# Kernel optimization log

Hardware: AMD Instinct MI355X
Metric: run time of the kernel (lower is better)

The kernel has to match this reference:

```python
import jax, jax.numpy as jnp
import numpy as np

B, N, IN_F, OUT_F, H, NUM_EDGE_TYPES = 16, 512, 256, 256, 8, 50
HEAD_DIM = OUT_F // H
LN_EPS = 1e-5


def setup_inputs() -> dict:
    key = jax.random.key(0)
    ks = jax.random.split(key, 8)
    x = jax.random.normal(ks[0], (B, N, IN_F), dtype=jnp.float32)
    adj = jax.random.randint(ks[1], (B, N, N), 0, 2, dtype=jnp.int32)
    edge_types = jax.random.randint(ks[2], (B, N, N), 0, NUM_EDGE_TYPES, dtype=jnp.int32)
    # Parameters (torch Linear stores weight as [out, in]; we keep [in, out] for x @ W)
    W = jax.random.normal(ks[3], (IN_F, OUT_F), dtype=jnp.float32) / np.sqrt(IN_F)
    a1 = jax.random.normal(ks[4], (HEAD_DIM,), dtype=jnp.float32) / np.sqrt(HEAD_DIM)
    a2 = jax.random.normal(ks[5], (HEAD_DIM,), dtype=jnp.float32) / np.sqrt(HEAD_DIM)
    edge_emb = jax.random.normal(ks[6], (NUM_EDGE_TYPES, H), dtype=jnp.float32) * 0.02
    edge_emb = edge_emb.at[0].set(0.0)  # padding_idx=0
    ln_gamma = jnp.ones((OUT_F,), dtype=jnp.float32)
    ln_beta = jnp.zeros((OUT_F,), dtype=jnp.float32)
    return {"x": x, "adj": adj, "edge_types": edge_types, "W": W, "a1": a1,
            "a2": a2, "edge_emb": edge_emb, "ln_gamma": ln_gamma, "ln_beta": ln_beta}


def reference(x, adj, edge_types, W, a1, a2, edge_emb, ln_gamma, ln_beta):
    Bx, Nx, _ = x.shape
    # Wh: [B, N, H, D]
    Wh = (x @ W).reshape(Bx, Nx, H, HEAD_DIM)
    # per-node attention scalars: [B, N, H]
    s1 = jnp.einsum('bnhd,d->bnh', Wh, a1)
    s2 = jnp.einsum('bnhd,d->bnh', Wh, a2)
    # e: [B, N(i), N(j), H]
    e = s1[:, :, None, :] + s2[:, None, :, :] + edge_emb[edge_types]
    e = jnp.where(e > 0, e, 0.2 * e)  # leaky_relu(0.2)
    e = jnp.where((adj == 0)[..., None], jnp.float32(-1e9), e)
    alpha = jax.nn.softmax(e, axis=2)  # softmax over j
    # (dropout omitted: eval mode / deterministic reference)
    h = jnp.einsum('bijh,bjhd->bihd', alpha, Wh).reshape(Bx, Nx, OUT_F)
    # LayerNorm over last dim
    mu = jnp.mean(h, axis=-1, keepdims=True)
    var = jnp.mean(jnp.square(h - mu), axis=-1, keepdims=True)
    hn = (h - mu) * jax.lax.rsqrt(var + LN_EPS) * ln_gamma + ln_beta
    return jax.nn.elu(hn)
```

## Files before the change

kernel.cpp:

```cpp
#include <hip/hip_runtime.h>
#include <hip/hip_bf16.h>
#include <stdint.h>

namespace gat {
constexpr int NB   = 16;
constexpr int NN   = 512;
constexpr int FIN  = 256;
constexpr int FOUT = 256;
constexpr int H    = 8;
constexpr int NE   = 50;
constexpr float L2E  = 1.4426950408889634f;
constexpr float MASKB = -192.0f;
constexpr float RBIAS = 0.00281502f;
}
using namespace gat;

typedef __attribute__((ext_vector_type(8))) short short8;
typedef __attribute__((ext_vector_type(4))) float f32x4;

__device__ __forceinline__ unsigned pk_bf16(unsigned ulo, unsigned uhi) {
  return __builtin_amdgcn_perm(uhi, ulo, 0x07060302u);
}
__device__ __forceinline__ unsigned pk2f(float a, float b) {
  return pk_bf16(__float_as_uint(a) + 0x8000u, __float_as_uint(b) + 0x8000u);
}
__device__ __forceinline__ unsigned short bf1(float a) {
  return (unsigned short)((__float_as_uint(a) + 0x8000u) >> 16);
}

__global__ __launch_bounds__(256) void k_prew(const float* __restrict__ Wm,
                                              const float* __restrict__ a1,
                                              const float* __restrict__ a2,
                                              unsigned short* __restrict__ WbTa) {
  const int blk = blockIdx.x;
  if (blk < 256) {
    const int k = blk;
    const int f = threadIdx.x;
    WbTa[f * FIN + k] = bf1(Wm[k * FOUT + f]);
  } else {
    const int k = threadIdx.x;
    const float* wr = Wm + (size_t)k * FOUT;
    #pragma unroll
    for (int h = 0; h < H; ++h) {
      float v1 = 0.f, v2 = 0.f;
      #pragma unroll
      for (int d = 0; d < 32; ++d) {
        const float wv = wr[h * 32 + d];
        v1 += wv * a1[d];
        v2 += wv * a2[d];
      }
      WbTa[(256 + h) * FIN + k] = bf1(v1);
      WbTa[(264 + h) * FIN + k] = bf1(v2);
    }
  }
}

__global__ __launch_bounds__(256, 4) void k_gp(
    const float* __restrict__ x, const unsigned short* __restrict__ WbTa,
    const int* __restrict__ adj, const int* __restrict__ ety,
    unsigned short* __restrict__ WhT, float* __restrict__ s1T, float* __restrict__ s2T,
    unsigned* __restrict__ codes)
{
  const int t = threadIdx.x;
  if (blockIdx.x >= 512) {
    const size_t base = ((size_t)(blockIdx.x - 512) * 256 + t) * 16;
    const int4* ap = (const int4*)(adj + base);
    const int4* ep = (const int4*)(ety + base);
    unsigned o[4];
    #pragma unroll
    for (int g = 0; g < 4; ++g) {
      const int4 a = ap[g];
      const int4 e = ep[g];
      o[g] = (unsigned)(e.x | (a.x << 6))
           | ((unsigned)(e.y | (a.y << 6)) << 8)
           | ((unsigned)(e.z | (a.z << 6)) << 16)
           | ((unsigned)(e.w | (a.w << 6)) << 24);
    }
    uint4 v; v.x = o[0]; v.y = o[1]; v.z = o[2]; v.w = o[3];
    *(uint4*)(codes + base / 4) = v;
    return;
  }

  __shared__ alignas(16) unsigned short xS[16 * 264];
  const int row0 = blockIdx.x * 16;
  {
    const int r  = t >> 4;
    const int kb = (t & 15) * 16;
    const float4* xg = (const float4*)(x + (size_t)(row0 + r) * FIN + kb);
    const float4 v0 = xg[0], v1 = xg[1], v2 = xg[2], v3 = xg[3];
    uint4 o0, o1;
    o0.x = pk2f(v0.x, v0.y); o0.y = pk2f(v0.z, v0.w);
    o0.z = pk2f(v1.x, v1.y); o0.w = pk2f(v1.z, v1.w);
    o1.x = pk2f(v2.x, v2.y); o1.y = pk2f(v2.z, v2.w);
    o1.z = pk2f(v3.x, v3.y); o1.w = pk2f(v3.z, v3.w);
    *(uint4*)&xS[r * 264 + kb]     = o0;
    *(uint4*)&xS[r * 264 + kb + 8] = o1;
  }
  __syncthreads();

  const int w    = t >> 6;
  const int L    = t & 63;
  const int nn   = L & 15;
  const int quad = L >> 4;
  const unsigned short* wb = WbTa + (size_t)(w * 64 + nn) * FIN + quad * 8;
  const unsigned short* wa = WbTa + (size_t)(256 + nn) * FIN + quad * 8;
  const unsigned short* xp = &xS[nn * 264 + quad * 8];

  f32x4 acc0 = {0.f,0.f,0.f,0.f}, acc1 = {0.f,0.f,0.f,0.f};
  f32x4 acc2 = {0.f,0.f,0.f,0.f}, acc3 = {0.f,0.f,0.f,0.f};
  f32x4 accA = {0.f,0.f,0.f,0.f};

  #pragma unroll
  for (int kc = 0; kc < 8; ++kc) {
    const int k0 = kc * 32;
    const short8 A  = *(const short8*)(xp + k0);
    const short8 B0 = *(const short8*)(wb + k0);
    const short8 B1 = *(const short8*)(wb + 16 * FIN + k0);
    const short8 B2 = *(const short8*)(wb + 32 * FIN + k0);
    const short8 B3 = *(const short8*)(wb + 48 * FIN + k0);
    acc0 = __builtin_amdgcn_mfma_f32_16x16x32_bf16(A, B0, acc0, 0, 0, 0);
    acc1 = __builtin_amdgcn_mfma_f32_16x16x32_bf16(A, B1, acc1, 0, 0, 0);
    acc2 = __builtin_amdgcn_mfma_f32_16x16x32_bf16(A, B2, acc2, 0, 0, 0);
    acc3 = __builtin_amdgcn_mfma_f32_16x16x32_bf16(A, B3, acc3, 0, 0, 0);
    if (w == 3) {
      const short8 BA = *(const short8*)(wa + k0);
      accA = __builtin_amdgcn_mfma_f32_16x16x32_bf16(A, BA, accA, 0, 0, 0);
    }
  }

  const int b     = row0 >> 9;
  const int node0 = (row0 & 511) + quad * 4;
  f32x4 accs[4] = {acc0, acc1, acc2, acc3};
  #pragma unroll
  for (int ft = 0; ft < 4; ++ft) {
    const int f = w * 64 + ft * 16 + nn;
    uint2 o;
    o.x = pk2f(accs[ft][0], accs[ft][1]);
    o.y = pk2f(accs[ft][2], accs[ft][3]);
    *(uint2*)(WhT + (size_t)((b * 8 + (f >> 5)) * 32 + (f & 31)) * 512 + node0) = o;
  }
  if (w == 3) {
    float4 sv;
    sv.x = accA[0] * L2E; sv.y = accA[1] * L2E;
    sv.z = accA[2] * L2E; sv.w = accA[3] * L2E;
    float* dst = (nn < 8) ? (s1T + (size_t)(b * 8 + nn) * 512 + node0)
                          : (s2T + (size_t)(b * 8 + (nn - 8)) * 512 + node0);
    *(float4*)dst = sv;
  }
}

__global__ __launch_bounds__(512, 4) void k_attn(
    const unsigned char* __restrict__ codes,
    const float* __restrict__ s1T, const float* __restrict__ s2T,
    const unsigned short* __restrict__ WhT, const float* __restrict__ emb,
    const float* __restrict__ gam, const float* __restrict__ bet,
    float* __restrict__ out)
{
  __shared__ float2 embS[4 * 128];
  __shared__ float2 lnS[16 * 4];
  __shared__ float  s2S[8 * 512];
  __shared__ float  redS[256 * 18];

  const int t    = threadIdx.x;
  const int b    = blockIdx.x >> 5;
  const int i0   = (blockIdx.x & 31) * 16;
  const int W    = t >> 6;
  const int w    = W & 3;
  const int jh   = W >> 2;
  const int L    = t & 63;
  const int i    = L & 15;
  const int quad = L >> 4;
  const int h0   = w, h1 = w + 4;

  {
    const float4* sg = (const float4*)(s2T + (size_t)b * 8 * 512);
    float4* ss = (float4*)s2S;
    ss[t]       = sg[t];
    ss[t + 512] = sg[t + 512];
  }
  {
    const int wp = t >> 7, c = t & 127;
    float2 v;
    if (c >= 64 && c < 64 + NE) {
      v.x = emb[(c - 64) * H + wp]     * L2E + RBIAS;
      v.y = emb[(c - 64) * H + wp + 4] * L2E + RBIAS;
    } else {
      v.x = MASKB; v.y = MASKB;
    }
    embS[t] = v;
  }

  const int row   = b * NN + i0 + i;
  const int jbase = jh * 256;
  uint2 cw[8];
  {
    const unsigned char* cp = codes + (size_t)row * NN + jbase + quad * 8;
    #pragma unroll
    for (int kc = 0; kc < 8; ++kc) cw[kc] = *(const uint2*)(cp + kc * 32);
  }
  const float si0 = s1T[(size_t)(b * 8 + h0) * 512 + i0 + i];
  const float si1 = s1T[(size_t)(b * 8 + h1) * 512 + i0 + i];
  const unsigned short* wt00 = WhT + (size_t)((b * 8 + h0) * 32 + i)      * 512;
  const unsigned short* wt01 = WhT + (size_t)((b * 8 + h0) * 32 + 16 + i) * 512;
  const unsigned short* wt10 = WhT + (size_t)((b * 8 + h1) * 32 + i)      * 512;
  const unsigned short* wt11 = WhT + (size_t)((b * 8 + h1) * 32 + 16 + i) * 512;

  f32x4 acc00 = {0.f,0.f,0.f,0.f}, acc01 = {0.f,0.f,0.f,0.f};
  f32x4 acc10 = {0.f,0.f,0.f,0.f}, acc11 = {0.f,0.f,0.f,0.f};
  f32x4 accL0 = {0.f,0.f,0.f,0.f}, accL1 = {0.f,0.f,0.f,0.f};
  const short one_bf = (short)0x3F80;
  const short8 ONES = {one_bf, one_bf, one_bf, one_bf, one_bf, one_bf, one_bf, one_bf};

  const int ja0 = jbase + quad * 8;
  short8 nA00 = *(const short8*)(wt00 + ja0);
  short8 nA01 = *(const short8*)(wt01 + ja0);
  short8 nA10 = *(const short8*)(wt10 + ja0);
  short8 nA11 = *(const short8*)(wt11 + ja0);

  __syncthreads();

  #pragma unroll
  for (int kc = 0; kc < 8; ++kc) {
    const int ja  = jbase + kc * 32 + quad * 8;
    const short8 A00 = nA00, A01 = nA01, A10 = nA10, A11 = nA11;
    {
      const int jn = ja + 32;
      nA00 = *(const short8*)(wt00 + jn);
      nA01 = *(const short8*)(wt01 + jn);
      nA10 = *(const short8*)(wt10 + jn);
      nA11 = *(const short8*)(wt11 + jn);
    }
    const float4 sa0 = *(const float4*)&s2S[h0 * 512 + ja];
    const float4 sb0 = *(const float4*)&s2S[h0 * 512 + ja + 4];
    const float4 sa1 = *(const float4*)&s2S[h1 * 512 + ja];
    const float4 sb1 = *(const float4*)&s2S[h1 * 512 + ja + 4];
    const float s20[8] = {sa0.x, sa0.y, sa0.z, sa0.w, sb0.x, sb0.y, sb0.z, sb0.w};
    const float s21[8] = {sa1.x, sa1.y, sa1.z, sa1.w, sb1.x, sb1.y, sb1.z, sb1.w};

    unsigned u0[8], u1[8];
    #pragma unroll
    for (int q = 0; q < 8; ++q) {
      const unsigned cword = (q < 4) ? cw[kc].x : cw[kc].y;
      const unsigned c = (cword >> ((q & 3) * 8)) & 0xffu;
      const float2 em = embS[w * 128 + c];
      float e0 = si0 + s20[q] + em.x;
      float e1 = si1 + s21[q] + em.y;
      e0 = fmaxf(e0, 0.2f * e0);
      e1 = fmaxf(e1, 0.2f * e1);
      u0[q] = __float_as_uint(exp2f(e0));
      u1[q] = __float_as_uint(exp2f(e1));
    }
    uint4 U0, U1;
    U0.x = pk_bf16(u0[0], u0[1]); U0.y = pk_bf16(u0[2], u0[3]);
    U0.z = pk_bf16(u0[4], u0[5]); U0.w = pk_bf16(u0[6], u0[7]);
    U1.x = pk_bf16(u1[0], u1[1]); U1.y = pk_bf16(u1[2], u1[3]);
    U1.z = pk_bf16(u1[4], u1[5]); U1.w = pk_bf16(u1[6], u1[7]);
    const short8 B0 = __builtin_bit_cast(short8, U0);
    const short8 B1 = __builtin_bit_cast(short8, U1);

    acc00 = __builtin_amdgcn_mfma_f32_16x16x32_bf16(A00, B0, acc00, 0, 0, 0);
    acc01 = __builtin_amdgcn_mfma_f32_16x16x32_bf16(A01, B0, acc01, 0, 0, 0);
    acc10 = __builtin_amdgcn_mfma_f32_16x16x32_bf16(A10, B1, acc10, 0, 0, 0);
    acc11 = __builtin_amdgcn_mfma_f32_16x16x32_bf16(A11, B1, acc11, 0, 0, 0);
    accL0 = __builtin_amdgcn_mfma_f32_16x16x32_bf16(ONES, B0, accL0, 0, 0, 0);
    accL1 = __builtin_amdgcn_mfma_f32_16x16x32_bf16(ONES, B1, accL1, 0, 0, 0);
  }

  const float l0 = accL0[0];
  const float l1 = accL1[0];

  const int tt = (w << 6) | L;
  if (jh == 1) {
    float* rp = redS + tt * 18;
    rp[0]=acc00[0]; rp[1]=acc00[1]; rp[2]=acc00[2]; rp[3]=acc00[3];
    rp[4]=acc01[0]; rp[5]=acc01[1]; rp[6]=acc01[2]; rp[7]=acc01[3];
    rp[8]=acc10[0]; rp[9]=acc10[1]; rp[10]=acc10[2]; rp[11]=acc10[3];
    rp[12]=acc11[0]; rp[13]=acc11[1]; rp[14]=acc11[2]; rp[15]=acc11[3];
    rp[16]=l0; rp[17]=l1;
  }
  __syncthreads();

  float vals[16]; float mu, rstd;
  if (jh == 0) {
    const float* rp = redS + tt * 18;
    acc00[0]+=rp[0]; acc00[1]+=rp[1]; acc00[2]+=rp[2]; acc00[3]+=rp[3];
    acc01[0]+=rp[4]; acc01[1]+=rp[5]; acc01[2]+=rp[6]; acc01[3]+=rp[7];
    acc10[0]+=rp[8]; acc10[1]+=rp[9]; acc10[2]+=rp[10]; acc10[3]+=rp[11];
    acc11[0]+=rp[12]; acc11[1]+=rp[13]; acc11[2]+=rp[14]; acc11[3]+=rp[15];
    const float inv0 = __builtin_amdgcn_rcpf(l0 + rp[16]);
    const float inv1 = __builtin_amdgcn_rcpf(l1 + rp[17]);
    #pragma unroll
    for (int r = 0; r < 4; ++r) {
      vals[r]      = acc00[r] * inv0;
      vals[4 + r]  = acc01[r] * inv0;
      vals[8 + r]  = acc10[r] * inv1;
      vals[12 + r] = acc11[r] * inv1;
    }
    float s = 0.f, ss = 0.f;
    #pragma unroll
    for (int k = 0; k < 16; ++k) { s += vals[k]; ss += vals[k] * vals[k]; }
    s += __shfl_xor(s, 16); ss += __shfl_xor(ss, 16);
    s += __shfl_xor(s, 32); ss += __shfl_xor(ss, 32);
    if (quad == 0) { float2 v; v.x = s; v.y = ss; lnS[i * 4 + w] = v; }
  }
  __syncthreads();
  if (jh == 1) return;
  {
    float S = 0.f, SS = 0.f;
    #pragma unroll
    for (int ww = 0; ww < 4; ++ww) { const float2 v = lnS[i * 4 + ww]; S += v.x; SS += v.y; }
    mu = S * (1.0f / 256.0f);
    const float var = SS * (1.0f / 256.0f) - mu * mu;
    rstd = rsqrtf(var + 1e-5f);
  }
  const int fb[4] = { h0 * 32 + quad * 4, h0 * 32 + 16 + quad * 4,
                      h1 * 32 + quad * 4, h1 * 32 + 16 + quad * 4 };
  #pragma unroll
  for (int g = 0; g < 4; ++g) {
    const float4 gv = *(const float4*)(gam + fb[g]);
    const float4 bv = *(const float4*)(bet + fb[g]);
    float4 o;
    o.x = (vals[g*4+0] - mu) * rstd * gv.x + bv.x;
    o.y = (vals[g*4+1] - mu) * rstd * gv.y + bv.y;
    o.z = (vals[g*4+2] - mu) * rstd * gv.z + bv.z;
    o.w = (vals[g*4+3] - mu) * rstd * gv.w + bv.w;
    o.x = o.x > 0.f ? o.x : exp2f(o.x * L2E) - 1.f;
    o.y = o.y > 0.f ? o.y : exp2f(o.y * L2E) - 1.f;
    o.z = o.z > 0.f ? o.z : exp2f(o.z * L2E) - 1.f;
    o.w = o.w > 0.f ? o.w : exp2f(o.w * L2E) - 1.f;
    *(float4*)(out + (size_t)row * FOUT + fb[g]) = o;
  }
}

extern "C" void kernel_launch(void* const* d_in, const int* in_sizes, int n_in,
                              void* d_out, int out_size, void* d_ws, size_t ws_size,
                              hipStream_t stream) {
  (void)in_sizes; (void)n_in; (void)out_size; (void)ws_size;
  const float* x   = (const float*)d_in[0];
  const int*   adj = (const int*)  d_in[1];
  const int*   ety = (const int*)  d_in[2];
  const float* Wm  = (const float*)d_in[3];
  const float* a1  = (const float*)d_in[4];
  const float* a2  = (const float*)d_in[5];
  const float* emb = (const float*)d_in[6];
  const float* gam = (const float*)d_in[7];
  const float* bet = (const float*)d_in[8];
  float* out = (float*)d_out;

  unsigned short* WhT  = (unsigned short*)d_ws;
  unsigned short* WbTa = WhT + (size_t)NB * H * 32 * 512;
  float* s1T  = (float*)(WbTa + (size_t)272 * FIN);
  float* s2T  = s1T + (size_t)NB * H * NN;
  unsigned char* codes = (unsigned char*)(s2T + (size_t)NB * H * NN);

  k_prew<<<dim3(257),  dim3(256), 0, stream>>>(Wm, a1, a2, WbTa);
  k_gp  <<<dim3(1536), dim3(256), 0, stream>>>(x, WbTa, adj, ety, WhT, s1T, s2T, (unsigned*)codes);
  k_attn<<<dim3(NB * (NN / 16)), dim3(512), 0, stream>>>(codes, s1T, s2T, WhT, emb, gam, bet, out);
}
```

Before: 138.4 us.

## Split attention j-range across four wave groups with tree reduction

The attention kernel now runs 1024 threads per block, splitting the neighbor (j) dimension four ways instead of two, so each wave processes 128 columns. Partial MFMA accumulators and softmax denominators are combined through a two-level shared-memory tree reduction with extra barriers. This aims to raise parallelism per block and hide latency. In exchange it adds reduction traffic and synchronisation, doubles the shared reduction buffer, and launch_bounds(1024,8) may force register spills.

```diff
diff --git a/kernel.cpp b/kernel.cpp
--- a/kernel.cpp
+++ b/kernel.cpp
@@ -149,7 +149,7 @@
   }
 }
 
-__global__ __launch_bounds__(512, 4) void k_attn(
+__global__ __launch_bounds__(1024, 8) void k_attn(
     const unsigned char* __restrict__ codes,
     const float* __restrict__ s1T, const float* __restrict__ s2T,
     const unsigned short* __restrict__ WhT, const float* __restrict__ emb,
@@ -159,26 +159,23 @@
   __shared__ float2 embS[4 * 128];
   __shared__ float2 lnS[16 * 4];
   __shared__ float  s2S[8 * 512];
-  __shared__ float  redS[256 * 18];
+  __shared__ float  redS[512 * 18];
 
   const int t    = threadIdx.x;
   const int b    = blockIdx.x >> 5;
   const int i0   = (blockIdx.x & 31) * 16;
   const int W    = t >> 6;
   const int w    = W & 3;
-  const int jh   = W >> 2;
+  const int jq   = W >> 2;
   const int L    = t & 63;
   const int i    = L & 15;
   const int quad = L >> 4;
   const int h0   = w, h1 = w + 4;
 
   {
-    const float4* sg = (const float4*)(s2T + (size_t)b * 8 * 512);
-    float4* ss = (float4*)s2S;
-    ss[t]       = sg[t];
-    ss[t + 512] = sg[t + 512];
-  }
-  {
+    ((float4*)s2S)[t] = ((const float4*)(s2T + (size_t)b * 8 * 512))[t];
+  }
+  if (t < 512) {
     const int wp = t >> 7, c = t & 127;
     float2 v;
     if (c >= 64 && c < 64 + NE) {
@@ -191,12 +188,12 @@
   }
 
   const int row   = b * NN + i0 + i;
-  const int jbase = jh * 256;
-  uint2 cw[8];
+  const int jbase = jq * 128;
+  uint2 cw[4];
   {
     const unsigned char* cp = codes + (size_t)row * NN + jbase + quad * 8;
     #pragma unroll
-    for (int kc = 0; kc < 8; ++kc) cw[kc] = *(const uint2*)(cp + kc * 32);
+    for (int kc = 0; kc < 4; ++kc) cw[kc] = *(const uint2*)(cp + kc * 32);
   }
   const float si0 = s1T[(size_t)(b * 8 + h0) * 512 + i0 + i];
   const float si1 = s1T[(size_t)(b * 8 + h1) * 512 + i0 + i];
@@ -220,7 +217,7 @@
   __syncthreads();
 
   #pragma unroll
-  for (int kc = 0; kc < 8; ++kc) {
+  for (int kc = 0; kc < 4; ++kc) {
     const int ja  = jbase + kc * 32 + quad * 8;
     const short8 A00 = nA00, A01 = nA01, A10 = nA10, A11 = nA11;
     {
@@ -266,12 +263,12 @@
     accL1 = __builtin_amdgcn_mfma_f32_16x16x32_bf16(ONES, B1, accL1, 0, 0, 0);
   }
 
-  const float l0 = accL0[0];
-  const float l1 = accL1[0];
+  float l0 = accL0[0];
+  float l1 = accL1[0];
 
   const int tt = (w << 6) | L;
-  if (jh == 1) {
-    float* rp = redS + tt * 18;
+  if (jq & 1) {
+    float* rp = redS + ((size_t)((jq >> 1) * 256 + tt)) * 18;
     rp[0]=acc00[0]; rp[1]=acc00[1]; rp[2]=acc00[2]; rp[3]=acc00[3];
     rp[4]=acc01[0]; rp[5]=acc01[1]; rp[6]=acc01[2]; rp[7]=acc01[3];
     rp[8]=acc10[0]; rp[9]=acc10[1]; rp[10]=acc10[2]; rp[11]=acc10[3];
@@ -279,10 +276,28 @@
     rp[16]=l0; rp[17]=l1;
   }
   __syncthreads();
-
-  float vals[16]; float mu, rstd;
-  if (jh == 0) {
-    const float* rp = redS + tt * 18;
+  if (!(jq & 1)) {
+    const float* rp = redS + ((size_t)((jq >> 1) * 256 + tt)) * 18;
+    acc00[0]+=rp[0]; acc00[1]+=rp[1]; acc00[2]+=rp[2]; acc00[3]+=rp[3];
+    acc01[0]+=rp[4]; acc01[1]+=rp[5]; acc01[2]+=rp[6]; acc01[3]+=rp[7];
+    acc10[0]+=rp[8]; acc10[1]+=rp[9]; acc10[2]+=rp[10]; acc10[3]+=rp[11];
+    acc11[0]+=rp[12]; acc11[1]+=rp[13]; acc11[2]+=rp[14]; acc11[3]+=rp[15];
+    l0 += rp[16]; l1 += rp[17];
+  }
+  __syncthreads();
+  if (jq == 2) {
+    float* rp = redS + (size_t)tt * 18;
+    rp[0]=acc00[0]; rp[1]=acc00[1]; rp[2]=acc00[2]; rp[3]=acc00[3];
+    rp[4]=acc01[0]; rp[5]=acc01[1]; rp[6]=acc01[2]; rp[7]=acc01[3];
+    rp[8]=acc10[0]; rp[9]=acc10[1]; rp[10]=acc10[2]; rp[11]=acc10[3];
+    rp[12]=acc11[0]; rp[13]=acc11[1]; rp[14]=acc11[2]; rp[15]=acc11[3];
+    rp[16]=l0; rp[17]=l1;
+  }
+  __syncthreads();
+
+  float vals[16];
+  if (jq == 0) {
+    const float* rp = redS + (size_t)tt * 18;
     acc00[0]+=rp[0]; acc00[1]+=rp[1]; acc00[2]+=rp[2]; acc00[3]+=rp[3];
     acc01[0]+=rp[4]; acc01[1]+=rp[5]; acc01[2]+=rp[6]; acc01[3]+=rp[7];
     acc10[0]+=rp[8]; acc10[1]+=rp[9]; acc10[2]+=rp[10]; acc10[3]+=rp[11];
@@ -304,7 +319,9 @@
     if (quad == 0) { float2 v; v.x = s; v.y = ss; lnS[i * 4 + w] = v; }
   }
   __syncthreads();
-  if (jh == 1) return;
+  if (jq != 0) return;
+
+  float mu, rstd;
   {
     float S = 0.f, SS = 0.f;
     #pragma unroll
@@ -355,5 +372,5 @@
 
   k_prew<<<dim3(257),  dim3(256), 0, stream>>>(Wm, a1, a2, WbTa);
   k_gp  <<<dim3(1536), dim3(256), 0, stream>>>(x, WbTa, adj, ety, WhT, s1T, s2T, (unsigned*)codes);
-  k_attn<<<dim3(NB * (NN / 16)), dim3(512), 0, stream>>>(codes, s1T, s2T, WhT, emb, gam, bet, out);
-}
+  k_attn<<<dim3(NB * (NN / 16)), dim3(1024), 0, stream>>>(codes, s1T, s2T, WhT, emb, gam, bet, out);
+}
```

Measured after the change: 158.9 us. +14.8%, slower.

## Split attention work so each wave handles one head, doubling block size

Applied to the files above, without the earlier changes.

The attention kernel now runs 16 waves per block, each handling a single head over half the neighbours, instead of 8 waves each handling two heads. This halves per-thread accumulators, edge-embedding lookups and exp work, so register use drops and occupancy can rise under the tighter launch bound. Edge codes are now prefetched one chunk ahead rather than all loaded up front. The software prefetch of the WhT operands is removed, and each code row is read by twice as many waves, which adds load traffic and latency exposure.

```diff
diff --git a/kernel.cpp b/kernel.cpp
--- a/kernel.cpp
+++ b/kernel.cpp
@@ -149,176 +149,130 @@
   }
 }
 
-__global__ __launch_bounds__(512, 4) void k_attn(
+__global__ __launch_bounds__(1024, 8) void k_attn(
     const unsigned char* __restrict__ codes,
     const float* __restrict__ s1T, const float* __restrict__ s2T,
     const unsigned short* __restrict__ WhT, const float* __restrict__ emb,
     const float* __restrict__ gam, const float* __restrict__ bet,
     float* __restrict__ out)
 {
-  __shared__ float2 embS[4 * 128];
-  __shared__ float2 lnS[16 * 4];
+  __shared__ float  embS[8 * 128];
+  __shared__ float2 lnS[16 * 8];
   __shared__ float  s2S[8 * 512];
-  __shared__ float  redS[256 * 18];
+  __shared__ float  redS[512 * 10];
 
   const int t    = threadIdx.x;
   const int b    = blockIdx.x >> 5;
   const int i0   = (blockIdx.x & 31) * 16;
   const int W    = t >> 6;
-  const int w    = W & 3;
-  const int jh   = W >> 2;
+  const int h    = W & 7;
+  const int jh   = W >> 3;
   const int L    = t & 63;
   const int i    = L & 15;
   const int quad = L >> 4;
-  const int h0   = w, h1 = w + 4;
-
+
+  ((float4*)s2S)[t] = ((const float4*)(s2T + (size_t)b * 8 * 512))[t];
   {
-    const float4* sg = (const float4*)(s2T + (size_t)b * 8 * 512);
-    float4* ss = (float4*)s2S;
-    ss[t]       = sg[t];
-    ss[t + 512] = sg[t + 512];
-  }
-  {
-    const int wp = t >> 7, c = t & 127;
-    float2 v;
-    if (c >= 64 && c < 64 + NE) {
-      v.x = emb[(c - 64) * H + wp]     * L2E + RBIAS;
-      v.y = emb[(c - 64) * H + wp + 4] * L2E + RBIAS;
-    } else {
-      v.x = MASKB; v.y = MASKB;
-    }
+    const int hp = t >> 7, c = t & 127;
+    float v = MASKB;
+    if (c >= 64 && c < 64 + NE) v = emb[(c - 64) * H + hp] * L2E + RBIAS;
     embS[t] = v;
   }
 
   const int row   = b * NN + i0 + i;
   const int jbase = jh * 256;
-  uint2 cw[8];
-  {
-    const unsigned char* cp = codes + (size_t)row * NN + jbase + quad * 8;
-    #pragma unroll
-    for (int kc = 0; kc < 8; ++kc) cw[kc] = *(const uint2*)(cp + kc * 32);
-  }
-  const float si0 = s1T[(size_t)(b * 8 + h0) * 512 + i0 + i];
-  const float si1 = s1T[(size_t)(b * 8 + h1) * 512 + i0 + i];
-  const unsigned short* wt00 = WhT + (size_t)((b * 8 + h0) * 32 + i)      * 512;
-  const unsigned short* wt01 = WhT + (size_t)((b * 8 + h0) * 32 + 16 + i) * 512;
-  const unsigned short* wt10 = WhT + (size_t)((b * 8 + h1) * 32 + i)      * 512;
-  const unsigned short* wt11 = WhT + (size_t)((b * 8 + h1) * 32 + 16 + i) * 512;
-
-  f32x4 acc00 = {0.f,0.f,0.f,0.f}, acc01 = {0.f,0.f,0.f,0.f};
-  f32x4 acc10 = {0.f,0.f,0.f,0.f}, acc11 = {0.f,0.f,0.f,0.f};
-  f32x4 accL0 = {0.f,0.f,0.f,0.f}, accL1 = {0.f,0.f,0.f,0.f};
+  const unsigned char* cp = codes + (size_t)row * NN + jbase + quad * 8;
+
+  const float si = s1T[(size_t)(b * 8 + h) * 512 + i0 + i];
+  const unsigned short* wt0 = WhT + (size_t)((b * 8 + h) * 32 + i)      * 512;
+  const unsigned short* wt1 = WhT + (size_t)((b * 8 + h) * 32 + 16 + i) * 512;
+  const float* s2p  = s2S + h * 512;
+  const float* embH = embS + h * 128;
+
+  f32x4 acc0 = {0.f,0.f,0.f,0.f}, acc1 = {0.f,0.f,0.f,0.f}, accL = {0.f,0.f,0.f,0.f};
   const short one_bf = (short)0x3F80;
   const short8 ONES = {one_bf, one_bf, one_bf, one_bf, one_bf, one_bf, one_bf, one_bf};
 
-  const int ja0 = jbase + quad * 8;
-  short8 nA00 = *(const short8*)(wt00 + ja0);
-  short8 nA01 = *(const short8*)(wt01 + ja0);
-  short8 nA10 = *(const short8*)(wt10 + ja0);
-  short8 nA11 = *(const short8*)(wt11 + ja0);
+  uint2 cwc = *(const uint2*)cp;
 
   __syncthreads();
 
   #pragma unroll
   for (int kc = 0; kc < 8; ++kc) {
-    const int ja  = jbase + kc * 32 + quad * 8;
-    const short8 A00 = nA00, A01 = nA01, A10 = nA10, A11 = nA11;
-    {
-      const int jn = ja + 32;
-      nA00 = *(const short8*)(wt00 + jn);
-      nA01 = *(const short8*)(wt01 + jn);
-      nA10 = *(const short8*)(wt10 + jn);
-      nA11 = *(const short8*)(wt11 + jn);
+    const int ja = jbase + kc * 32 + quad * 8;
+    uint2 cwn;
+    if (kc < 7) cwn = *(const uint2*)(cp + (kc + 1) * 32);
+    const short8 A0 = *(const short8*)(wt0 + ja);
+    const short8 A1 = *(const short8*)(wt1 + ja);
+    const float4 sa = *(const float4*)&s2p[ja];
+    const float4 sb = *(const float4*)&s2p[ja + 4];
+    const float s2v[8] = {sa.x, sa.y, sa.z, sa.w, sb.x, sb.y, sb.z, sb.w};
+
+    unsigned u[8];
+    #pragma unroll
+    for (int q = 0; q < 8; ++q) {
+      const unsigned cword = (q < 4) ? cwc.x : cwc.y;
+      const unsigned c = (cword >> ((q & 3) * 8)) & 0xffu;
+      float e = si + s2v[q] + embH[c];
+      e = fmaxf(e, 0.2f * e);
+      u[q] = __float_as_uint(exp2f(e));
     }
-    const float4 sa0 = *(const float4*)&s2S[h0 * 512 + ja];
-    const float4 sb0 = *(const float4*)&s2S[h0 * 512 + ja + 4];
-    const float4 sa1 = *(const float4*)&s2S[h1 * 512 + ja];
-    const float4 sb1 = *(const float4*)&s2S[h1 * 512 + ja + 4];
-    const float s20[8] = {sa0.x, sa0.y, sa0.z, sa0.w, sb0.x, sb0.y, sb0.z, sb0.w};
-    const float s21[8] = {sa1.x, sa1.y, sa1.z, sa1.w, sb1.x, sb1.y, sb1.z, sb1.w};
-
-    unsigned u0[8], u1[8];
-    #pragma unroll
-    for (int q = 0; q < 8; ++q) {
-      const unsigned cword = (q < 4) ? cw[kc].x : cw[kc].y;
-      const unsigned c = (cword >> ((q & 3) * 8)) & 0xffu;
-      const float2 em = embS[w * 128 + c];
-      float e0 = si0 + s20[q] + em.x;
-      float e1 = si1 + s21[q] + em.y;
-      e0 = fmaxf(e0, 0.2f * e0);
-      e1 = fmaxf(e1, 0.2f * e1);
-      u0[q] = __float_as_uint(exp2f(e0));
-      u1[q] = __float_as_uint(exp2f(e1));
-    }
-    uint4 U0, U1;
-    U0.x = pk_bf16(u0[0], u0[1]); U0.y = pk_bf16(u0[2], u0[3]);
-    U0.z = pk_bf16(u0[4], u0[5]); U0.w = pk_bf16(u0[6], u0[7]);
-    U1.x = pk_bf16(u1[0], u1[1]); U1.y = pk_bf16(u1[2], u1[3]);
-    U1.z = pk_bf16(u1[4], u1[5]); U1.w = pk_bf16(u1[6], u1[7]);
-    const short8 B0 = __builtin_bit_cast(short8, U0);
-    const short8 B1 = __builtin_bit_cast(short8, U1);
-
-    acc00 = __builtin_amdgcn_mfma_f32_16x16x32_bf16(A00, B0, acc00, 0, 0, 0);
-    acc01 = __builtin_amdgcn_mfma_f32_16x16x32_bf16(A01, B0, acc01, 0, 0, 0);
-    acc10 = __builtin_amdgcn_mfma_f32_16x16x32_bf16(A10, B1, acc10, 0, 0, 0);
-    acc11 = __builtin_amdgcn_mfma_f32_16x16x32_bf16(A11, B1, acc11, 0, 0, 0);
-    accL0 = __builtin_amdgcn_mfma_f32_16x16x32_bf16(ONES, B0, accL0, 0, 0, 0);
-    accL1 = __builtin_amdgcn_mfma_f32_16x16x32_bf16(ONES, B1, accL1, 0, 0, 0);
-  }
-
-  const float l0 = accL0[0];
-  const float l1 = accL1[0];
-
-  const int tt = (w << 6) | L;
+    uint4 U;
+    U.x = pk_bf16(u[0], u[1]); U.y = pk_bf16(u[2], u[3]);
+    U.z = pk_bf16(u[4], u[5]); U.w = pk_bf16(u[6], u[7]);
+    const short8 B = __builtin_bit_cast(short8, U);
+
+    acc0 = __builtin_amdgcn_mfma_f32_16x16x32_bf16(A0, B, acc0, 0, 0, 0);
+    acc1 = __builtin_amdgcn_mfma_f32_16x16x32_bf16(A1, B, acc1, 0, 0, 0);
+    accL = __builtin_amdgcn_mfma_f32_16x16x32_bf16(ONES, B, accL, 0, 0, 0);
+    cwc = cwn;
+  }
+
+  float l = accL[0];
+
+  const int slot = (h << 6) | L;
   if (jh == 1) {
-    float* rp = redS + tt * 18;
-    rp[0]=acc00[0]; rp[1]=acc00[1]; rp[2]=acc00[2]; rp[3]=acc00[3];
-    rp[4]=acc01[0]; rp[5]=acc01[1]; rp[6]=acc01[2]; rp[7]=acc01[3];
-    rp[8]=acc10[0]; rp[9]=acc10[1]; rp[10]=acc10[2]; rp[11]=acc10[3];
-    rp[12]=acc11[0]; rp[13]=acc11[1]; rp[14]=acc11[2]; rp[15]=acc11[3];
-    rp[16]=l0; rp[17]=l1;
+    float* rp = redS + slot * 10;
+    rp[0]=acc0[0]; rp[1]=acc0[1]; rp[2]=acc0[2]; rp[3]=acc0[3];
+    rp[4]=acc1[0]; rp[5]=acc1[1]; rp[6]=acc1[2]; rp[7]=acc1[3];
+    rp[8]=l;
   }
   __syncthreads();
 
-  float vals[16]; float mu, rstd;
+  float vals[8];
   if (jh == 0) {
-    const float* rp = redS + tt * 18;
-    acc00[0]+=rp[0]; acc00[1]+=rp[1]; acc00[2]+=rp[2]; acc00[3]+=rp[3];
-    acc01[0]+=rp[4]; acc01[1]+=rp[5]; acc01[2]+=rp[6]; acc01[3]+=rp[7];
-    acc10[0]+=rp[8]; acc10[1]+=rp[9]; acc10[2]+=rp[10]; acc10[3]+=rp[11];
-    acc11[0]+=rp[12]; acc11[1]+=rp[13]; acc11[2]+=rp[14]; acc11[3]+=rp[15];
-    const float inv0 = __builtin_amdgcn_rcpf(l0 + rp[16]);
-    const float inv1 = __builtin_amdgcn_rcpf(l1 + rp[17]);
-    #pragma unroll
-    for (int r = 0; r < 4; ++r) {
-      vals[r]      = acc00[r] * inv0;
-      vals[4 + r]  = acc01[r] * inv0;
-      vals[8 + r]  = acc10[r] * inv1;
-      vals[12 + r] = acc11[r] * inv1;
-    }
+    const float* rp = redS + slot * 10;
+    acc0[0]+=rp[0]; acc0[1]+=rp[1]; acc0[2]+=rp[2]; acc0[3]+=rp[3];
+    acc1[0]+=rp[4]; acc1[1]+=rp[5]; acc1[2]+=rp[6]; acc1[3]+=rp[7];
+    l += rp[8];
+    const float inv = __builtin_amdgcn_rcpf(l);
+    #pragma unroll
+    for (int r = 0; r < 4; ++r) { vals[r] = acc0[r] * inv; vals[4 + r] = acc1[r] * inv; }
     float s = 0.f, ss = 0.f;
     #pragma unroll
-    for (int k = 0; k < 16; ++k) { s += vals[k]; ss += vals[k] * vals[k]; }
+    for (int k = 0; k < 8; ++k) { s += vals[k]; ss += vals[k] * vals[k]; }
     s += __shfl_xor(s, 16); ss += __shfl_xor(ss, 16);
     s += __shfl_xor(s, 32); ss += __shfl_xor(ss, 32);
-    if (quad == 0) { float2 v; v.x = s; v.y = ss; lnS[i * 4 + w] = v; }
+    if (quad == 0) { float2 v; v.x = s; v.y = ss; lnS[i * 8 + h] = v; }
   }
   __syncthreads();
   if (jh == 1) return;
+
+  float mu, rstd;
   {
     float S = 0.f, SS = 0.f;
     #pragma unroll
-    for (int ww = 0; ww < 4; ++ww) { const float2 v = lnS[i * 4 + ww]; S += v.x; SS += v.y; }
+    for (int hh = 0; hh < 8; ++hh) { const float2 v = lnS[i * 8 + hh]; S += v.x; SS += v.y; }
     mu = S * (1.0f / 256.0f);
     const float var = SS * (1.0f / 256.0f) - mu * mu;
     rstd = rsqrtf(var + 1e-5f);
   }
-  const int fb[4] = { h0 * 32 + quad * 4, h0 * 32 + 16 + quad * 4,
-                      h1 * 32 + quad * 4, h1 * 32 + 16 + quad * 4 };
+  const int fb0 = h * 32 + quad * 4;
   #pragma unroll
-  for (int g = 0; g < 4; ++g) {
-    const float4 gv = *(const float4*)(gam + fb[g]);
-    const float4 bv = *(const float4*)(bet + fb[g]);
+  for (int g = 0; g < 2; ++g) {
+    const int fb = fb0 + g * 16;
+    const float4 gv = *(const float4*)(gam + fb);
+    const float4 bv = *(const float4*)(bet + fb);
     float4 o;
     o.x = (vals[g*4+0] - mu) * rstd * gv.x + bv.x;
     o.y = (vals[g*4+1] - mu) * rstd * gv.y + bv.y;
@@ -328,7 +282,7 @@
     o.y = o.y > 0.f ? o.y : exp2f(o.y * L2E) - 1.f;
     o.z = o.z > 0.f ? o.z : exp2f(o.z * L2E) - 1.f;
     o.w = o.w > 0.f ? o.w : exp2f(o.w * L2E) - 1.f;
-    *(float4*)(out + (size_t)row * FOUT + fb[g]) = o;
+    *(float4*)(out + (size_t)row * FOUT + fb) = o;
   }
 }
 
@@ -355,5 +309,5 @@
 
   k_prew<<<dim3(257),  dim3(256), 0, stream>>>(Wm, a1, a2, WbTa);
   k_gp  <<<dim3(1536), dim3(256), 0, stream>>>(x, WbTa, adj, ety, WhT, s1T, s2T, (unsigned*)codes);
-  k_attn<<<dim3(NB * (NN / 16)), dim3(512), 0, stream>>>(codes, s1T, s2T, WhT, emb, gam, bet, out);
-}
+  k_attn<<<dim3(NB * (NN / 16)), dim3(1024), 0, stream>>>(codes, s1T, s2T, WhT, emb, gam, bet, out);
+}
```

New measurement: 140.4 us. About the same (+1.4%).
